# Optimization experiments

Hardware: AMD Instinct MI355X
Metric: run time of the kernel (lower is better)

## Reference

```python
import jax, jax.numpy as jnp
import numpy as np

N_NODES = 50000
N_EDGES = 800000
IN_CH, HID_CH, OUT_CH = 128, 256, 128


def setup_inputs() -> dict:
    key = jax.random.key(0)
    k1, k2, k3, k4 = jax.random.split(key, 4)
    x = jax.random.normal(k1, (N_NODES, IN_CH), dtype=jnp.float32)
    edge_index = jax.random.randint(k2, (2, N_EDGES), 0, N_NODES, dtype=jnp.int32)
    # Glorot-ish scaled weights
    W1 = jax.random.normal(k3, (IN_CH, HID_CH), dtype=jnp.float32) * (1.0 / np.sqrt(IN_CH))
    b1 = jnp.zeros((HID_CH,), dtype=jnp.float32)
    W2 = jax.random.normal(k4, (HID_CH, OUT_CH), dtype=jnp.float32) * (1.0 / np.sqrt(HID_CH))
    b2 = jnpp = jnp.zeros((OUT_CH,), dtype=jnp.float32)
    return {"x": x, "edge_index": edge_index, "W1": W1, "b1": b1, "W2": W2, "b2": b2}


def _gcn_conv(x, W, b, src, dst, num_nodes):
    """PyG GCNConv: add self-loops, symmetric deg^-1/2 norm, linear, scatter-add."""
    h = x @ W  # [N, out] dense transform first (as in GCNConv)
    # in-degree including self-loops (edge weights = 1)
    deg = jax.ops.segment_sum(jnp.ones_like(dst, dtype=h.dtype), dst, num_segments=num_nodes)
    deg = deg + 1.0  # self-loop contribution
    dinv = jnp.where(deg > 0, jax.lax.rsqrt(deg), 0.0)
    # neighbor messages: norm_e * h[src_e], scatter-added to dst
    norm = dinv[src] * dinv[dst]                      # [E]
    msg = h[src] * norm[:, None]                      # [E, out] gather
    agg = jax.ops.segment_sum(msg, dst, num_segments=num_nodes)  # scatter-add
    # self-loop messages: dinv[i]^2 * h[i]
    agg = agg + h * (dinv * dinv)[:, None]
    return agg + b


def reference(x, edge_index, W1, b1, W2, b2):
    src, dst = edge_index[0], edge_index[1]
    n = x.shape[0]
    h = jax.nn.relu(_gcn_conv(x, W1, b1, src, dst, n))
    return _gcn_conv(h, W2, b2, src, dst, n)
```

## Files before the change

### kernel.cpp

```cpp
#include <hip/hip_runtime.h>

#define N_NODES 50000
#define N_EDGES 800000
#define IN_CH 128
#define HID_CH 256
#define OUT_CH 128
#define BUCKET 64

#define N_XCD 8
#define NODES_PER_XCD 6250

using half8 = __attribute__((ext_vector_type(8))) _Float16;
using f32x4 = __attribute__((ext_vector_type(4))) float;


#define FILL_CHUNKS 3125
#define FILL_BLOCKS (FILL_CHUNKS * N_XCD)
#define CVT_BLOCKS 3125
#define WT1_BLOCKS 256
#define WT2_BLOCKS 128

__global__ __launch_bounds__(256) void prep_kernel(const int* __restrict__ src,
                                                   const int* __restrict__ dst,
                                                   int* __restrict__ cnt,
                                                   unsigned short* __restrict__ bucket,
                                                   const float* __restrict__ x,
                                                   _Float16* __restrict__ x16,
                                                   const float* __restrict__ W1,
                                                   _Float16* __restrict__ W1T,
                                                   const float* __restrict__ W2,
                                                   _Float16* __restrict__ W2T) {
    int b = blockIdx.x, t = threadIdx.x;
    if (b < FILL_BLOCKS) {
        int g = b & 7;
        int chunk = b >> 3;
        int i = chunk * 256 + t;
        if (i < N_EDGES) {
            int d = dst[i];
            int lo = g * NODES_PER_XCD;
            if (d >= lo && d < lo + NODES_PER_XCD) {
                int s = src[i];
                int p = atomicAdd(&cnt[d], 1);
                if (p < BUCKET) bucket[(size_t)d * BUCKET + p] = (unsigned short)s;
            }
        }
    } else if (b < FILL_BLOCKS + CVT_BLOCKS) {
        int i = (b - FILL_BLOCKS) * 256 + t;
        float4 v0 = ((const float4*)x)[i * 2];
        float4 v1 = ((const float4*)x)[i * 2 + 1];
        half8 o = {(_Float16)v0.x, (_Float16)v0.y, (_Float16)v0.z, (_Float16)v0.w,
                   (_Float16)v1.x, (_Float16)v1.y, (_Float16)v1.z, (_Float16)v1.w};
        ((half8*)x16)[i] = o;
    } else if (b < FILL_BLOCKS + CVT_BLOCKS + WT1_BLOCKS) {
        int n = b - FILL_BLOCKS - CVT_BLOCKS;
        if (t < IN_CH) W1T[(size_t)n * IN_CH + t] = (_Float16)W1[(size_t)t * HID_CH + n];
    } else {
        int n = b - FILL_BLOCKS - CVT_BLOCKS - WT1_BLOCKS;
        if (t < HID_CH) W2T[(size_t)n * HID_CH + t] = (_Float16)W2[(size_t)t * OUT_CH + n];
    }
}


template <bool OUT16>
__global__ __launch_bounds__(256) void agg16_kernel(const _Float16* __restrict__ h16,
                                                    const int* __restrict__ cnt,
                                                    const unsigned short* __restrict__ bucket,
                                                    const float* __restrict__ bias,
                                                    void* __restrict__ outp) {
    int t = blockIdx.x * 256 + threadIdx.x;
    int v = t >> 4;
    int sub = t & 15;
    int deg = cnt[v];
    float dv = rsqrtf((float)deg + 1.0f);
    half8 hv = ((const half8*)(h16 + (size_t)v * 128))[sub];
    float acc[8];
#pragma unroll
    for (int i = 0; i < 8; i++) acc[i] = (float)hv[i] * dv * dv;

    const unsigned short* bk = bucket + (size_t)v * BUCKET;
    for (int base = 0; base < deg; base += 16) {
        int idx = base + sub;
        int a = 0;
        float c = 0.f;
        if (idx < deg) {
            a = bk[idx];
            c = rsqrtf((float)cnt[a] + 1.0f) * dv;
        }
        int len = min(deg - base, 16);
        int j = 0;
        for (; j + 8 <= len; j += 8) {
            int   s0 = __shfl(a, j + 0, 16); float w0 = __shfl(c, j + 0, 16);
            int   s1 = __shfl(a, j + 1, 16); float w1 = __shfl(c, j + 1, 16);
            int   s2 = __shfl(a, j + 2, 16); float w2 = __shfl(c, j + 2, 16);
            int   s3 = __shfl(a, j + 3, 16); float w3 = __shfl(c, j + 3, 16);
            int   s4 = __shfl(a, j + 4, 16); float w4 = __shfl(c, j + 4, 16);
            int   s5 = __shfl(a, j + 5, 16); float w5 = __shfl(c, j + 5, 16);
            int   s6 = __shfl(a, j + 6, 16); float w6 = __shfl(c, j + 6, 16);
            int   s7 = __shfl(a, j + 7, 16); float w7 = __shfl(c, j + 7, 16);
            half8 x0 = ((const half8*)(h16 + (size_t)s0 * 128))[sub];
            half8 x1 = ((const half8*)(h16 + (size_t)s1 * 128))[sub];
            half8 x2 = ((const half8*)(h16 + (size_t)s2 * 128))[sub];
            half8 x3 = ((const half8*)(h16 + (size_t)s3 * 128))[sub];
            half8 x4 = ((const half8*)(h16 + (size_t)s4 * 128))[sub];
            half8 x5 = ((const half8*)(h16 + (size_t)s5 * 128))[sub];
            half8 x6 = ((const half8*)(h16 + (size_t)s6 * 128))[sub];
            half8 x7 = ((const half8*)(h16 + (size_t)s7 * 128))[sub];
#pragma unroll
            for (int i = 0; i < 8; i++) acc[i] += w0 * (float)x0[i];
#pragma unroll
            for (int i = 0; i < 8; i++) acc[i] += w1 * (float)x1[i];
#pragma unroll
            for (int i = 0; i < 8; i++) acc[i] += w2 * (float)x2[i];
#pragma unroll
            for (int i = 0; i < 8; i++) acc[i] += w3 * (float)x3[i];
#pragma unroll
            for (int i = 0; i < 8; i++) acc[i] += w4 * (float)x4[i];
#pragma unroll
            for (int i = 0; i < 8; i++) acc[i] += w5 * (float)x5[i];
#pragma unroll
            for (int i = 0; i < 8; i++) acc[i] += w6 * (float)x6[i];
#pragma unroll
            for (int i = 0; i < 8; i++) acc[i] += w7 * (float)x7[i];
        }
        for (; j + 4 <= len; j += 4) {
            int   s0 = __shfl(a, j + 0, 16); float w0 = __shfl(c, j + 0, 16);
            int   s1 = __shfl(a, j + 1, 16); float w1 = __shfl(c, j + 1, 16);
            int   s2 = __shfl(a, j + 2, 16); float w2 = __shfl(c, j + 2, 16);
            int   s3 = __shfl(a, j + 3, 16); float w3 = __shfl(c, j + 3, 16);
            half8 x0 = ((const half8*)(h16 + (size_t)s0 * 128))[sub];
            half8 x1 = ((const half8*)(h16 + (size_t)s1 * 128))[sub];
            half8 x2 = ((const half8*)(h16 + (size_t)s2 * 128))[sub];
            half8 x3 = ((const half8*)(h16 + (size_t)s3 * 128))[sub];
#pragma unroll
            for (int i = 0; i < 8; i++) acc[i] += w0 * (float)x0[i];
#pragma unroll
            for (int i = 0; i < 8; i++) acc[i] += w1 * (float)x1[i];
#pragma unroll
            for (int i = 0; i < 8; i++) acc[i] += w2 * (float)x2[i];
#pragma unroll
            for (int i = 0; i < 8; i++) acc[i] += w3 * (float)x3[i];
        }
        for (; j < len; j++) {
            int   s = __shfl(a, j, 16);
            float w = __shfl(c, j, 16);
            half8 xv = ((const half8*)(h16 + (size_t)s * 128))[sub];
#pragma unroll
            for (int i = 0; i < 8; i++) acc[i] += w * (float)xv[i];
        }
    }

    if (OUT16) {
        half8 o;
#pragma unroll
        for (int i = 0; i < 8; i++) o[i] = (_Float16)acc[i];
        ((half8*)outp)[(size_t)v * 16 + sub] = o;
    } else {
        const float4* bp = (const float4*)bias;
        float4 b0 = bp[sub * 2], b1v = bp[sub * 2 + 1];
        float4 o0 = make_float4(acc[0] + b0.x, acc[1] + b0.y, acc[2] + b0.z, acc[3] + b0.w);
        float4 o1 = make_float4(acc[4] + b1v.x, acc[5] + b1v.y, acc[6] + b1v.z, acc[7] + b1v.w);
        float4* op = (float4*)outp;
        op[(size_t)v * 32 + sub * 2] = o0;
        op[(size_t)v * 32 + sub * 2 + 1] = o1;
    }
}


template <int BM, bool EPI>
__global__ __launch_bounds__(256) void mfma_gemm_kernel(const _Float16* __restrict__ A,
                                                        const _Float16* __restrict__ BT,
                                                        const float* __restrict__ bias,
                                                        _Float16* __restrict__ C,
                                                        int M, int N, int K) {
    const int MT = BM / 32;
    const int LDA = 40;
    const int SMEM = (BM * 136 * 2 > (BM + 128) * 80) ? BM * 136 * 2 : (BM + 128) * 80;
    __shared__ __align__(16) char smem[SMEM];
    _Float16* As = (_Float16*)smem;
    _Float16* Bs = (_Float16*)(smem + BM * 80);
    _Float16* Cs = (_Float16*)smem;

    int tid = threadIdx.x;
    int wave = tid >> 6, lane = tid & 63;
    int quad = lane >> 4, l16 = lane & 15;
    int wm = wave >> 1, wn = wave & 1;
    int bm = blockIdx.y * BM, bn = blockIdx.x * 128;

    f32x4 acc[MT][4] = {};

    for (int k0 = 0; k0 < K; k0 += 32) {
#pragma unroll
        for (int q = tid; q < BM * 4; q += 256) {
            int row = q >> 2, seg = q & 3;
            int gr = bm + row;
            float4 v = make_float4(0.f, 0.f, 0.f, 0.f);
            if (gr < M) v = *(const float4*)(A + (size_t)gr * K + k0 + seg * 8);
            *(float4*)(As + row * LDA + seg * 8) = v;
        }
#pragma unroll
        for (int q = tid; q < 512; q += 256) {
            int row = q >> 2, seg = q & 3;
            float4 v = *(const float4*)(BT + (size_t)(bn + row) * K + k0 + seg * 8);
            *(float4*)(Bs + row * LDA + seg * 8) = v;
        }
        __syncthreads();
        half8 af[MT], bf[4];
#pragma unroll
        for (int mt = 0; mt < MT; mt++)
            af[mt] = *(const half8*)(As + (wm * (BM / 2) + mt * 16 + l16) * LDA + quad * 8);
#pragma unroll
        for (int nt = 0; nt < 4; nt++)
            bf[nt] = *(const half8*)(Bs + (wn * 64 + nt * 16 + l16) * LDA + quad * 8);
#pragma unroll
        for (int mt = 0; mt < MT; mt++)
#pragma unroll
            for (int nt = 0; nt < 4; nt++)
                acc[mt][nt] = __builtin_amdgcn_mfma_f32_16x16x32_f16(af[mt], bf[nt], acc[mt][nt], 0, 0, 0);
        __syncthreads();
    }

#pragma unroll
    for (int mt = 0; mt < MT; mt++) {
#pragma unroll
        for (int nt = 0; nt < 4; nt++) {
#pragma unroll
            for (int r = 0; r < 4; r++) {
                int ml = wm * (BM / 2) + mt * 16 + quad * 4 + r;
                int nl = wn * 64 + nt * 16 + l16;
                float v = acc[mt][nt][r];
                if (EPI) {
                    v += bias[bn + nl];
                    v = fmaxf(v, 0.f);
                }
                Cs[ml * 136 + nl] = (_Float16)v;
            }
        }
    }
    __syncthreads();
#pragma unroll
    for (int q = tid; q < BM * 16; q += 256) {
        int row = q >> 4, seg = q & 15;
        int gr = bm + row;
        if (gr < M)
            *(float4*)(C + (size_t)gr * N + bn + seg * 8) = *(const float4*)(Cs + row * 136 + seg * 8);
    }
}


extern "C" void kernel_launch(void* const* d_in, const int* in_sizes, int n_in,
                              void* d_out, int out_size, void* d_ws, size_t ws_size,
                              hipStream_t stream) {
    const float* x  = (const float*)d_in[0];
    const int*   ei = (const int*)d_in[1];
    const int*   src = ei;
    const int*   dst = ei + N_EDGES;
    const float* W1 = (const float*)d_in[2];
    const float* b1 = (const float*)d_in[3];
    const float* W2 = (const float*)d_in[4];
    const float* b2 = (const float*)d_in[5];
    float* out = (float*)d_out;

    char* w = (char*)d_ws;
    auto alloc = [&](size_t bytes) -> void* {
        void* p = (void*)w;
        w += (bytes + 255) & ~(size_t)255;
        return p;
    };
    int*            cnt    = (int*)alloc((size_t)N_NODES * 4);
    unsigned short* bucket = (unsigned short*)alloc((size_t)N_NODES * BUCKET * 2);
    _Float16*       x16    = (_Float16*)alloc((size_t)N_NODES * IN_CH * 2);
    _Float16*       a1     = (_Float16*)alloc((size_t)N_NODES * IN_CH * 2);
    _Float16*       h1     = (_Float16*)alloc((size_t)N_NODES * HID_CH * 2);
    _Float16*       t2     = (_Float16*)alloc((size_t)N_NODES * OUT_CH * 2);
    _Float16*       W1T    = (_Float16*)alloc((size_t)IN_CH * HID_CH * 2);
    _Float16*       W2T    = (_Float16*)alloc((size_t)HID_CH * OUT_CH * 2);

    hipMemsetAsync(cnt, 0, (size_t)N_NODES * 4, stream);

    prep_kernel<<<FILL_BLOCKS + CVT_BLOCKS + WT1_BLOCKS + WT2_BLOCKS, 256, 0, stream>>>(
        src, dst, cnt, bucket, x, x16, W1, W1T, W2, W2T);

    agg16_kernel<true><<<N_NODES * 16 / 256, 256, 0, stream>>>(x16, cnt, bucket, nullptr, a1);
    dim3 g1(HID_CH / 128, (N_NODES + 127) / 128);
    mfma_gemm_kernel<128, true><<<g1, 256, 0, stream>>>(a1, W1T, b1, h1, N_NODES, HID_CH, IN_CH);

    dim3 g2(OUT_CH / 128, (N_NODES + 63) / 64);
    mfma_gemm_kernel<64, false><<<g2, 256, 0, stream>>>(h1, W2T, nullptr, t2, N_NODES, OUT_CH, HID_CH);
    agg16_kernel<false><<<N_NODES * 16 / 256, 256, 0, stream>>>(t2, cnt, bucket, b2, out);
}
```

Measured before the change: 226.0 us.

## Fuse both GEMMs into one kernel keeping hidden activations in shared memory

The two separate MFMA GEMM launches are replaced by one fused kernel. Each 64-row block computes relu(A·W1+b1) into LDS and immediately multiplies it by W2, so the 50000×256 fp16 hidden tensor is never written to or read back from global memory. In exchange, the larger LDS footprint (about 68 KB per block) may lower occupancy, and W1/W2 tiles are reloaded by every block. The aggregation kernel also clamps its loop count to the bucket capacity, which bounds the neighbour loop.

```diff
diff --git a/kernel.cpp b/kernel.cpp
--- a/kernel.cpp
+++ b/kernel.cpp
@@ -70,8 +70,8 @@
     int t = blockIdx.x * 256 + threadIdx.x;
     int v = t >> 4;
     int sub = t & 15;
-    int deg = cnt[v];
-    float dv = rsqrtf((float)deg + 1.0f);
+    int deg = min(cnt[v], BUCKET);
+    float dv = rsqrtf((float)cnt[v] + 1.0f);
     half8 hv = ((const half8*)(h16 + (size_t)v * 128))[sub];
     float acc[8];
 #pragma unroll
@@ -166,83 +166,108 @@
 }
 
 
-template <int BM, bool EPI>
-__global__ __launch_bounds__(256) void mfma_gemm_kernel(const _Float16* __restrict__ A,
-                                                        const _Float16* __restrict__ BT,
-                                                        const float* __restrict__ bias,
-                                                        _Float16* __restrict__ C,
-                                                        int M, int N, int K) {
-    const int MT = BM / 32;
-    const int LDA = 40;
-    const int SMEM = (BM * 136 * 2 > (BM + 128) * 80) ? BM * 136 * 2 : (BM + 128) * 80;
-    __shared__ __align__(16) char smem[SMEM];
-    _Float16* As = (_Float16*)smem;
-    _Float16* Bs = (_Float16*)(smem + BM * 80);
-    _Float16* Cs = (_Float16*)smem;
+__global__ __launch_bounds__(256) void fused_mlp_kernel(const _Float16* __restrict__ A,
+                                                        const _Float16* __restrict__ W1T,
+                                                        const float* __restrict__ b1,
+                                                        const _Float16* __restrict__ W2T,
+                                                        _Float16* __restrict__ T2, int M) {
+    const int LDH = 264;
+    const int LDA = 136;
+    const int LDB = 40;
+    __shared__ __align__(16) _Float16 h1s[64 * LDH];
+    __shared__ __align__(16) _Float16 As[64 * LDA];
+    __shared__ __align__(16) _Float16 Bs[128 * LDB];
 
     int tid = threadIdx.x;
     int wave = tid >> 6, lane = tid & 63;
     int quad = lane >> 4, l16 = lane & 15;
     int wm = wave >> 1, wn = wave & 1;
-    int bm = blockIdx.y * BM, bn = blockIdx.x * 128;
-
-    f32x4 acc[MT][4] = {};
-
-    for (int k0 = 0; k0 < K; k0 += 32) {
-#pragma unroll
-        for (int q = tid; q < BM * 4; q += 256) {
-            int row = q >> 2, seg = q & 3;
-            int gr = bm + row;
-            float4 v = make_float4(0.f, 0.f, 0.f, 0.f);
-            if (gr < M) v = *(const float4*)(A + (size_t)gr * K + k0 + seg * 8);
-            *(float4*)(As + row * LDA + seg * 8) = v;
-        }
-#pragma unroll
+    int bm = blockIdx.x * 64;
+
+    for (int q = tid; q < 64 * 16; q += 256) {
+        int row = q >> 4, seg = q & 15;
+        int gr = bm + row;
+        float4 v = make_float4(0.f, 0.f, 0.f, 0.f);
+        if (gr < M) v = *(const float4*)(A + (size_t)gr * IN_CH + seg * 8);
+        *(float4*)(As + row * LDA + seg * 8) = v;
+    }
+
+    for (int nh = 0; nh < 2; nh++) {
+        f32x4 acc[2][4] = {};
+        for (int k0 = 0; k0 < IN_CH; k0 += 32) {
+            for (int q = tid; q < 512; q += 256) {
+                int row = q >> 2, seg = q & 3;
+                float4 v = *(const float4*)(W1T + (size_t)(nh * 128 + row) * IN_CH + k0 + seg * 8);
+                *(float4*)(Bs + row * LDB + seg * 8) = v;
+            }
+            __syncthreads();
+            half8 af[2], bf[4];
+#pragma unroll
+            for (int mt = 0; mt < 2; mt++)
+                af[mt] = *(const half8*)(As + (wm * 32 + mt * 16 + l16) * LDA + k0 + quad * 8);
+#pragma unroll
+            for (int nt = 0; nt < 4; nt++)
+                bf[nt] = *(const half8*)(Bs + (wn * 64 + nt * 16 + l16) * LDB + quad * 8);
+#pragma unroll
+            for (int mt = 0; mt < 2; mt++)
+#pragma unroll
+                for (int nt = 0; nt < 4; nt++)
+                    acc[mt][nt] = __builtin_amdgcn_mfma_f32_16x16x32_f16(af[mt], bf[nt], acc[mt][nt], 0, 0, 0);
+            __syncthreads();
+        }
+#pragma unroll
+        for (int mt = 0; mt < 2; mt++)
+#pragma unroll
+            for (int nt = 0; nt < 4; nt++)
+#pragma unroll
+                for (int r = 0; r < 4; r++) {
+                    int ml = wm * 32 + mt * 16 + quad * 4 + r;
+                    int nl = wn * 64 + nt * 16 + l16;
+                    float v = acc[mt][nt][r] + b1[nh * 128 + nl];
+                    h1s[ml * LDH + nh * 128 + nl] = (_Float16)fmaxf(v, 0.f);
+                }
+    }
+
+    f32x4 acc2[2][4] = {};
+    for (int k0 = 0; k0 < HID_CH; k0 += 32) {
         for (int q = tid; q < 512; q += 256) {
             int row = q >> 2, seg = q & 3;
-            float4 v = *(const float4*)(BT + (size_t)(bn + row) * K + k0 + seg * 8);
-            *(float4*)(Bs + row * LDA + seg * 8) = v;
+            float4 v = *(const float4*)(W2T + (size_t)row * HID_CH + k0 + seg * 8);
+            *(float4*)(Bs + row * LDB + seg * 8) = v;
         }
         __syncthreads();
-        half8 af[MT], bf[4];
-#pragma unroll
-        for (int mt = 0; mt < MT; mt++)
-            af[mt] = *(const half8*)(As + (wm * (BM / 2) + mt * 16 + l16) * LDA + quad * 8);
+        half8 af[2], bf[4];
+#pragma unroll
+        for (int mt = 0; mt < 2; mt++)
+            af[mt] = *(const half8*)(h1s + (wm * 32 + mt * 16 + l16) * LDH + k0 + quad * 8);
 #pragma unroll
         for (int nt = 0; nt < 4; nt++)
-            bf[nt] = *(const half8*)(Bs + (wn * 64 + nt * 16 + l16) * LDA + quad * 8);
-#pragma unroll
-        for (int mt = 0; mt < MT; mt++)
+            bf[nt] = *(const half8*)(Bs + (wn * 64 + nt * 16 + l16) * LDB + quad * 8);
+#pragma unroll
+        for (int mt = 0; mt < 2; mt++)
 #pragma unroll
             for (int nt = 0; nt < 4; nt++)
-                acc[mt][nt] = __builtin_amdgcn_mfma_f32_16x16x32_f16(af[mt], bf[nt], acc[mt][nt], 0, 0, 0);
+                acc2[mt][nt] = __builtin_amdgcn_mfma_f32_16x16x32_f16(af[mt], bf[nt], acc2[mt][nt], 0, 0, 0);
         __syncthreads();
     }
 
-#pragma unroll
-    for (int mt = 0; mt < MT; mt++) {
-#pragma unroll
-        for (int nt = 0; nt < 4; nt++) {
+    _Float16* Cs = As;
+#pragma unroll
+    for (int mt = 0; mt < 2; mt++)
+#pragma unroll
+        for (int nt = 0; nt < 4; nt++)
 #pragma unroll
             for (int r = 0; r < 4; r++) {
-                int ml = wm * (BM / 2) + mt * 16 + quad * 4 + r;
+                int ml = wm * 32 + mt * 16 + quad * 4 + r;
                 int nl = wn * 64 + nt * 16 + l16;
-                float v = acc[mt][nt][r];
-                if (EPI) {
-                    v += bias[bn + nl];
-                    v = fmaxf(v, 0.f);
-                }
-                Cs[ml * 136 + nl] = (_Float16)v;
+                Cs[ml * LDA + nl] = (_Float16)acc2[mt][nt][r];
             }
-        }
-    }
     __syncthreads();
-#pragma unroll
-    for (int q = tid; q < BM * 16; q += 256) {
+    for (int q = tid; q < 64 * 16; q += 256) {
         int row = q >> 4, seg = q & 15;
         int gr = bm + row;
         if (gr < M)
-            *(float4*)(C + (size_t)gr * N + bn + seg * 8) = *(const float4*)(Cs + row * 136 + seg * 8);
+            *(float4*)(T2 + (size_t)gr * OUT_CH + seg * 8) = *(const float4*)(Cs + row * LDA + seg * 8);
     }
 }
 
@@ -270,7 +295,6 @@
     unsigned short* bucket = (unsigned short*)alloc((size_t)N_NODES * BUCKET * 2);
     _Float16*       x16    = (_Float16*)alloc((size_t)N_NODES * IN_CH * 2);
     _Float16*       a1     = (_Float16*)alloc((size_t)N_NODES * IN_CH * 2);
-    _Float16*       h1     = (_Float16*)alloc((size_t)N_NODES * HID_CH * 2);
     _Float16*       t2     = (_Float16*)alloc((size_t)N_NODES * OUT_CH * 2);
     _Float16*       W1T    = (_Float16*)alloc((size_t)IN_CH * HID_CH * 2);
     _Float16*       W2T    = (_Float16*)alloc((size_t)HID_CH * OUT_CH * 2);
@@ -281,10 +305,6 @@
         src, dst, cnt, bucket, x, x16, W1, W1T, W2, W2T);
 
     agg16_kernel<true><<<N_NODES * 16 / 256, 256, 0, stream>>>(x16, cnt, bucket, nullptr, a1);
-    dim3 g1(HID_CH / 128, (N_NODES + 127) / 128);
-    mfma_gemm_kernel<128, true><<<g1, 256, 0, stream>>>(a1, W1T, b1, h1, N_NODES, HID_CH, IN_CH);
-
-    dim3 g2(OUT_CH / 128, (N_NODES + 63) / 64);
-    mfma_gemm_kernel<64, false><<<g2, 256, 0, stream>>>(h1, W2T, nullptr, t2, N_NODES, OUT_CH, HID_CH);
+    fused_mlp_kernel<<<(N_NODES + 63) / 64, 256, 0, stream>>>(a1, W1T, b1, W2T, t2, N_NODES);
     agg16_kernel<false><<<N_NODES * 16 / 256, 256, 0, stream>>>(t2, cnt, bucket, b2, out);
 }
```

New measurement: 217.5 us. 1.04x faster.
